# Kernel tuning notes

Measured on AMD Instinct MI355X. Metric: run time of the kernel, lower is better.

Reference implementation:

```python
import jax, jax.numpy as jnp
import numpy as np

N_NODES = 100000


def gcn_conv(x, edge_index, W, b):
    # PyG GCNConv: add self-loops, symmetric normalization, then scatter-add.
    n = x.shape[0]
    loops = jnp.arange(n, dtype=edge_index.dtype)
    src = jnp.concatenate([edge_index[0], loops])
    dst = jnp.concatenate([edge_index[1], loops])
    h = x @ W  # [N, F_out] -- transform before propagate (small GEMM)
    ones = jnp.ones(src.shape[0], dtype=x.dtype)
    deg = jax.ops.segment_sum(ones, dst, num_segments=n)  # in-degree incl. self-loop
    dinv = jnp.where(deg > 0, jax.lax.rsqrt(deg), 0.0)
    norm = dinv[src] * dinv[dst]  # [E+N]
    msg = h[src] * norm[:, None]  # gather + scale, [E+N, F_out]
    out = jax.ops.segment_sum(msg, dst, num_segments=n)  # scatter-add
    return out + b


def setup_inputs() -> dict:
    key = jax.random.key(0)
    k1, k2, k3, k4 = jax.random.split(key, 4)
    d = 128
    x = jax.random.normal(k1, (N_NODES, d), dtype=jnp.float32)
    edge_index = jax.random.randint(k2, (2, 1600000), 0, N_NODES, dtype=jnp.int64)
    scale = 1.0 / np.sqrt(d)
    W1 = jax.random.normal(k3, (d, d), dtype=jnp.float32) * scale
    b1 = jnp.zeros((d,), dtype=jnp.float32)
    W2 = jax.random.normal(k4, (d, d), dtype=jnp.float32) * scale
    b2 = jnp.zeros((d,), dtype=jnp.float32)
    return {"x": x, "edge_index": edge_index, "W1": W1, "b1": b1, "W2": W2, "b2": b2}


def reference(x, edge_index, W1, b1, W2, b2):
    # Layer 1: GCNConv -> relu -> dropout(eval: identity)
    h = jax.nn.relu(gcn_conv(x, edge_index, W1, b1))
    # Layer 2
    h = jax.nn.relu(gcn_conv(h, edge_index, W2, b2))
    return h
```

## Files before the change

kernel.cpp:

```cpp
#include <hip/hip_runtime.h>


#define NFEAT 128
#define BSH 7
#define MAXNB 1024
#define BCAP 4096
#define HP 72
#define YP 132
#define CH2 2048
#define CLCAP 2064

typedef __attribute__((ext_vector_type(8))) short s8v;
typedef __attribute__((ext_vector_type(4))) float f4v;
typedef __attribute__((ext_vector_type(2))) float f2v;
typedef __attribute__((ext_vector_type(4))) uint u4v;

__device__ inline ushort f2bf(float f) {
    union { float f; uint u; } x; x.f = f;
    uint u = x.u;
    return (ushort)((u + 0x7fffu + ((u >> 16) & 1u)) >> 16);
}
__device__ inline f2v unpk(uint u) {
    union { uint u; float f; } lo, hi;
    lo.u = u << 16;
    hi.u = u & 0xffff0000u;
    return (f2v){lo.f, hi.f};
}
__device__ inline void upadd2(uint4 v, f2v* a) {
    a[0] += unpk(v.x);
    a[1] += unpk(v.y);
    a[2] += unpk(v.z);
    a[3] += unpk(v.w);
}

__device__ inline void node_gather_lds(const uint4* __restrict__ hs4,
                                       const int* colL, int s, int e,
                                       int node, int sub, f2v* a) {
    uint4 vself = hs4[(size_t)node * 16 + sub];
    int nb = (e - s) >> 2;
    int k = s;
    if (nb > 0) {
        int c0 = colL[k], c1 = colL[k + 1], c2 = colL[k + 2], c3 = colL[k + 3];
        uint4 v0 = hs4[(size_t)c0 * 16 + sub];
        uint4 v1 = hs4[(size_t)c1 * 16 + sub];
        uint4 v2 = hs4[(size_t)c2 * 16 + sub];
        uint4 v3 = hs4[(size_t)c3 * 16 + sub];
        int d0 = colL[k + 4], d1 = colL[k + 5], d2 = colL[k + 6], d3 = colL[k + 7];
        k += 8;
        upadd2(vself, a);
        for (int it = 1; it < nb; ++it, k += 4) {
            uint4 w0 = hs4[(size_t)d0 * 16 + sub];
            uint4 w1 = hs4[(size_t)d1 * 16 + sub];
            uint4 w2 = hs4[(size_t)d2 * 16 + sub];
            uint4 w3 = hs4[(size_t)d3 * 16 + sub];
            int t0 = colL[k], t1 = colL[k + 1], t2 = colL[k + 2], t3 = colL[k + 3];
            upadd2(v0, a); upadd2(v1, a); upadd2(v2, a); upadd2(v3, a);
            v0 = w0; v1 = w1; v2 = w2; v3 = w3;
            d0 = t0; d1 = t1; d2 = t2; d3 = t3;
        }
        upadd2(v0, a); upadd2(v1, a); upadd2(v2, a); upadd2(v3, a);
        k = s + nb * 4;
    } else {
        upadd2(vself, a);
    }
    for (; k < e; ++k) upadd2(hs4[(size_t)colL[k] * 16 + sub], a);
}

__device__ inline void half_sort(const uint* __restrict__ ebuf,
                                 const int* __restrict__ gcnt,
                                 int b, int half, int* cnt, int* sstart, int* pre,
                                 int* colL) {
    int t = threadIdx.x;
    int m = min(gcnt[b], BCAP);
    const uint* eb = ebuf + (size_t)b * BCAP;
    if (t < 64) cnt[t] = 0;
    __syncthreads();
    for (int i = t; i < m; i += 256) {
        int low = (int)(eb[i] & 127u);
        if ((low >> 6) == half) atomicAdd(&cnt[low & 63], 1);
    }
    __syncthreads();
    if (t < 64) {
        int v = cnt[t];
        int sc = v;
#pragma unroll
        for (int off = 1; off < 64; off <<= 1) {
            int u = __shfl_up(sc, off, 64);
            if (t >= off) sc += u;
        }
        sstart[t] = sc - v;
        pre[t] = sc - v;
    }
    __syncthreads();
    for (int i = t; i < m; i += 256) {
        uint p = eb[i];
        int low = (int)(p & 127u);
        if ((low >> 6) == half) {
            int pos = atomicAdd(&pre[low & 63], 1);
            if (pos < 2048) colL[pos] = (int)(p >> BSH);
        }
    }
    __syncthreads();
}

__device__ inline void stage_w_half(ushort* Bs, const float* __restrict__ W, int h, int t) {
#pragma unroll
    for (int i = 0; i < 8; i++) {
        int idx = t + i * 256;
        int k4 = idx >> 7;
        int n = idx & 127;
        ushort o[4];
#pragma unroll
        for (int j = 0; j < 4; j++) o[j] = f2bf(W[(h * 64 + k4 * 4 + j) * NFEAT + n]);
        uint2 pk;
        __builtin_memcpy(&pk, o, 8);
        *(uint2*)&Bs[n * HP + k4 * 4] = pk;
    }
}

__global__ __launch_bounds__(256) void k_deg(const int* __restrict__ dst,
                                             int* __restrict__ deg, int E) {
    int i = blockIdx.x * 256 + threadIdx.x;
    int stride = gridDim.x * 256;
    int E4 = E >> 2;
    const int4* d4 = (const int4*)dst;
    for (int k = i; k < E4; k += stride) {
        int4 v = d4[k];
        atomicAdd(&deg[v.x], 1);
        atomicAdd(&deg[v.y], 1);
        atomicAdd(&deg[v.z], 1);
        atomicAdd(&deg[v.w], 1);
    }
    for (int k = E4 * 4 + i; k < E; k += stride) atomicAdd(&deg[dst[k]], 1);
}

__device__ inline void bsort_body(char* smem, int sid,
                                  const int* __restrict__ src,
                                  const int* __restrict__ dst,
                                  int* __restrict__ gcnt,
                                  uint* __restrict__ ebuf, int E, int NB) {
    int* cnt_ = (int*)smem;
    int* loff = cnt_ + MAXNB;
    int* gbase = loff + MAXNB;
    int* wpart = gbase + MAXNB;
    uint* sv = (uint*)(wpart + 4);
    ushort* sb = (ushort*)(sv + CH2);

    int t = threadIdx.x;
    int e0 = sid * CH2;
    int m = min(CH2, E - e0);

#pragma unroll
    for (int i = t; i < MAXNB; i += 256) cnt_[i] = 0;
    __syncthreads();
    for (int e = e0 + t; e < e0 + m; e += 256) atomicAdd(&cnt_[dst[e] >> BSH], 1);
    __syncthreads();
    for (int b = t; b < NB; b += 256) {
        int c = cnt_[b];
        gbase[b] = c ? (b * BCAP + atomicAdd(&gcnt[b], c)) : 0;
    }
    int v0 = cnt_[t * 4], v1 = cnt_[t * 4 + 1], v2 = cnt_[t * 4 + 2], v3 = cnt_[t * 4 + 3];
    int my = v0 + v1 + v2 + v3;
    int lane = t & 63, wv = t >> 6;
    int sc = my;
#pragma unroll
    for (int off = 1; off < 64; off <<= 1) {
        int up = __shfl_up(sc, off, 64);
        if (lane >= off) sc += up;
    }
    if (lane == 63) wpart[wv] = sc;
    __syncthreads();
    int wbase = 0;
    for (int j = 0; j < wv; j++) wbase += wpart[j];
    int run = wbase + sc - my;
    loff[t * 4] = run; cnt_[t * 4] = run; run += v0;
    loff[t * 4 + 1] = run; cnt_[t * 4 + 1] = run; run += v1;
    loff[t * 4 + 2] = run; cnt_[t * 4 + 2] = run; run += v2;
    loff[t * 4 + 3] = run; cnt_[t * 4 + 3] = run;
    __syncthreads();
    for (int e = e0 + t; e < e0 + m; e += 256) {
        int d = dst[e];
        int b = d >> BSH;
        int p = atomicAdd(&cnt_[b], 1);
        sv[p] = ((uint)src[e] << BSH) | (uint)(d & ((1 << BSH) - 1));
        sb[p] = (ushort)b;
    }
    __syncthreads();
    for (int i = t; i < m; i += 256) {
        int b = sb[i];
        int slot = gbase[b] + (i - loff[b]);
        if (slot < (b + 1) * BCAP) ebuf[slot] = sv[i];
    }
}

__device__ inline void gemm_body_f32(ushort* Bs, int bid, const float* __restrict__ Ap,
                                     const float* __restrict__ W,
                                     const int* __restrict__ deg,
                                     ushort* __restrict__ hs, int M) {
    int t = threadIdx.x;
    int w = t >> 6, l = t & 63;
    int q = l >> 4, ln = l & 15;
    int row0 = (bid * 4 + w) * 16;

    int arow = row0 + ln;
    if (arow >= M) arow = M - 1;
    s8v afr[4];
    const float* A = Ap + (size_t)arow * NFEAT + q * 8;
#pragma unroll
    for (int g = 0; g < 4; g++) {
        float4 f0 = *(const float4*)(A + g * 32);
        float4 f1 = *(const float4*)(A + g * 32 + 4);
        ushort o[8] = {f2bf(f0.x), f2bf(f0.y), f2bf(f0.z), f2bf(f0.w),
                       f2bf(f1.x), f2bf(f1.y), f2bf(f1.z), f2bf(f1.w)};
        __builtin_memcpy(&afr[g], o, 16);
    }

    f4v acc[8];
#pragma unroll
    for (int nt = 0; nt < 8; nt++) acc[nt] = (f4v){0.f, 0.f, 0.f, 0.f};

#pragma unroll
    for (int h = 0; h < 2; h++) {
        if (h) __syncthreads();
        stage_w_half(Bs, W, h, t);
        __syncthreads();
#pragma unroll
        for (int nt = 0; nt < 8; nt++) {
            const ushort* Bp = Bs + (nt * 16 + ln) * HP + q * 8;
#pragma unroll
            for (int ks = 0; ks < 2; ks++) {
                s8v bfr = *(const s8v*)(Bp + ks * 32);
                acc[nt] = __builtin_amdgcn_mfma_f32_16x16x32_bf16(afr[h * 2 + ks], bfr, acc[nt], 0, 0, 0);
            }
        }
    }

#pragma unroll
    for (int r = 0; r < 4; r++) {
        int row = row0 + q * 4 + r;
        if (row < M) {
            float sc = rsqrtf((float)(deg[row] + 1));
            ushort* hp = hs + (size_t)row * NFEAT + ln;
#pragma unroll
            for (int nt = 0; nt < 8; nt++) hp[nt * 16] = f2bf(acc[nt][r] * sc);
        }
    }
}

__global__ __launch_bounds__(256) void k_fusedA(const int* __restrict__ src,
                                                const int* __restrict__ dst,
                                                int* __restrict__ gcnt,
                                                uint* __restrict__ ebuf,
                                                int E, int NB, int chBlk,
                                                const float* __restrict__ x,
                                                const float* __restrict__ W1,
                                                const int* __restrict__ deg,
                                                ushort* __restrict__ hs, int M) {
    __shared__ __align__(16) char smem[24592];
    int bid = blockIdx.x;
    int sid = bid / 3, r = bid % 3;
    if (r == 0 && sid < chBlk) {
        bsort_body(smem, sid, src, dst, gcnt, ebuf, E, NB);
    } else {
        int sorts_before = min(sid + (r ? 1 : 0), chBlk);
        gemm_body_f32((ushort*)smem, bid - sorts_before, x, W1, deg, hs, M);
    }
}

__global__ __launch_bounds__(256, 4) void k_aggB1(const uint4* __restrict__ hs4,
                                                  const uint* __restrict__ ebuf,
                                                  const int* __restrict__ gcnt,
                                                  const float* __restrict__ bias,
                                                  const float* __restrict__ W2,
                                                  ushort* __restrict__ hs2, int N) {
    __shared__ __align__(16) char smem[36096];
    ushort* yT = (ushort*)smem;
    char* scr = smem + 16896;
    int* cnt = (int*)(smem + 35328);
    int* sstart = (int*)(smem + 35584);
    int* pre = (int*)(smem + 35840);
    int* colL = (int*)scr;
    ushort* Bs = (ushort*)scr;

    int t = threadIdx.x;
    int b = blockIdx.x >> 1, half = blockIdx.x & 1;
    int base = (b << BSH) + half * 64;

    half_sort(ebuf, gcnt, b, half, cnt, sstart, pre, colL);

    int grp = t >> 4, sub = t & 15;
    const float4* b4 = (const float4*)bias;
    float4 bb0 = b4[sub * 2], bb1 = b4[sub * 2 + 1];

    for (int i = 0; i < 4; i++) {
        int lo = grp + i * 16;
        int node = base + lo;
        uint4 pk = make_uint4(0, 0, 0, 0);
        if (node < N) {
            f2v a[4];
#pragma unroll
            for (int j = 0; j < 4; j++) a[j] = (f2v){0.f, 0.f};
            int s = sstart[lo];
            int e = min(s + cnt[lo], 2048);
            node_gather_lds(hs4, colL, s, e, node, sub, a);
            float di = rsqrtf((float)(cnt[lo] + 1));
            ushort o[8];
            o[0] = f2bf(fmaxf(fmaf(di, a[0].x, bb0.x), 0.f));
            o[1] = f2bf(fmaxf(fmaf(di, a[0].y, bb0.y), 0.f));
            o[2] = f2bf(fmaxf(fmaf(di, a[1].x, bb0.z), 0.f));
            o[3] = f2bf(fmaxf(fmaf(di, a[1].y, bb0.w), 0.f));
            o[4] = f2bf(fmaxf(fmaf(di, a[2].x, bb1.x), 0.f));
            o[5] = f2bf(fmaxf(fmaf(di, a[2].y, bb1.y), 0.f));
            o[6] = f2bf(fmaxf(fmaf(di, a[3].x, bb1.z), 0.f));
            o[7] = f2bf(fmaxf(fmaf(di, a[3].y, bb1.w), 0.f));
            __builtin_memcpy(&pk, o, 16);
        }
        *(uint4*)&yT[lo * YP + sub * 8] = pk;
    }
    __syncthreads();

    int w = t >> 6, l = t & 63;
    int q = l >> 4, ln = l & 15;
    s8v a2[4];
#pragma unroll
    for (int g = 0; g < 4; g++)
        a2[g] = *(const s8v*)&yT[(w * 16 + ln) * YP + g * 32 + q * 8];

    f4v acc[8];
#pragma unroll
    for (int nt = 0; nt < 8; nt++) acc[nt] = (f4v){0.f, 0.f, 0.f, 0.f};
#pragma unroll
    for (int h = 0; h < 2; h++) {
        if (h) __syncthreads();
        stage_w_half(Bs, W2, h, t);
        __syncthreads();
#pragma unroll
        for (int nt = 0; nt < 8; nt++) {
            const ushort* Bp = Bs + (nt * 16 + ln) * HP + q * 8;
#pragma unroll
            for (int ks = 0; ks < 2; ks++) {
                s8v bfr = *(const s8v*)(Bp + ks * 32);
                acc[nt] = __builtin_amdgcn_mfma_f32_16x16x32_bf16(a2[h * 2 + ks], bfr, acc[nt], 0, 0, 0);
            }
        }
    }
#pragma unroll
    for (int rr = 0; rr < 4; rr++) {
        int lrow = w * 16 + q * 4 + rr;
        int node = base + lrow;
        if (node < N) {
            float sc = rsqrtf((float)(cnt[lrow] + 1));
            ushort* hp = hs2 + (size_t)node * NFEAT + ln;
#pragma unroll
            for (int nt = 0; nt < 8; nt++) hp[nt * 16] = f2bf(acc[nt][rr] * sc);
        }
    }
}

__global__ __launch_bounds__(256, 6) void k_aggB2(const uint4* __restrict__ hs4,
                                                  const uint* __restrict__ ebuf,
                                                  const int* __restrict__ gcnt,
                                                  const float* __restrict__ bias,
                                                  float* __restrict__ outp, int N) {
    __shared__ int cnt[64];
    __shared__ int sstart[64];
    __shared__ int pre[64];
    __shared__ int colL[CLCAP];

    int t = threadIdx.x;
    int b = blockIdx.x >> 1, half = blockIdx.x & 1;
    int base = (b << BSH) + half * 64;

    half_sort(ebuf, gcnt, b, half, cnt, sstart, pre, colL);

    int grp = t >> 4, sub = t & 15;
    const float4* b4 = (const float4*)bias;
    float4 bb0 = b4[sub * 2], bb1 = b4[sub * 2 + 1];

    for (int i = 0; i < 4; i++) {
        int lo = grp + i * 16;
        int node = base + lo;
        if (node >= N) continue;
        f2v a[4];
#pragma unroll
        for (int j = 0; j < 4; j++) a[j] = (f2v){0.f, 0.f};
        int s = sstart[lo];
        int e = min(s + cnt[lo], 2048);
        node_gather_lds(hs4, colL, s, e, node, sub, a);
        float di = rsqrtf((float)(cnt[lo] + 1));
        float r[8];
        r[0] = fmaxf(fmaf(di, a[0].x, bb0.x), 0.f);
        r[1] = fmaxf(fmaf(di, a[0].y, bb0.y), 0.f);
        r[2] = fmaxf(fmaf(di, a[1].x, bb0.z), 0.f);
        r[3] = fmaxf(fmaf(di, a[1].y, bb0.w), 0.f);
        r[4] = fmaxf(fmaf(di, a[2].x, bb1.x), 0.f);
        r[5] = fmaxf(fmaf(di, a[2].y, bb1.y), 0.f);
        r[6] = fmaxf(fmaf(di, a[3].x, bb1.z), 0.f);
        r[7] = fmaxf(fmaf(di, a[3].y, bb1.w), 0.f);
        float* orow = outp + (size_t)node * NFEAT + sub * 8;
        f4v r0 = {r[0], r[1], r[2], r[3]};
        f4v r1 = {r[4], r[5], r[6], r[7]};
        __builtin_nontemporal_store(r0, (f4v*)orow);
        __builtin_nontemporal_store(r1, (f4v*)(orow + 4));
    }
}

extern "C" void kernel_launch(void* const* d_in, const int* in_sizes, int n_in,
                              void* d_out, int out_size, void* d_ws, size_t ws_size,
                              hipStream_t stream) {
    const float* x = (const float*)d_in[0];
    const int* ei = (const int*)d_in[1];
    const float* W1 = (const float*)d_in[2];
    const float* b1 = (const float*)d_in[3];
    const float* W2 = (const float*)d_in[4];
    const float* b2 = (const float*)d_in[5];
    float* out = (float*)d_out;

    const int N = in_sizes[0] / NFEAT;
    const int E = in_sizes[1] / 2;
    const int* src = ei;
    const int* dst = ei + E;
    const int NB = (N + (1 << BSH) - 1) >> BSH;

    char* w = (char*)d_ws;
    size_t off = 0;
    auto alloc = [&](size_t bytes) -> void* {
        void* p = w + off;
        off = (off + bytes + 511) & ~(size_t)511;
        return p;
    };
    ushort* hs = (ushort*)alloc((size_t)N * NFEAT * 2);
    ushort* hs2 = (ushort*)alloc((size_t)N * NFEAT * 2);
    int* deg = (int*)alloc((size_t)N * 4);
    uint* ebuf = (uint*)alloc((size_t)NB * BCAP * 4);
    int* gcnt = (int*)alloc((size_t)MAXNB * 4);
    (void)ws_size; (void)n_in; (void)out_size;

    const int sortBlk = (E + CH2 - 1) / CH2;
    const int gemmBlk = (N + 63) / 64;
    const int aggBlk = 2 * NB;

    hipMemsetAsync(deg, 0, (size_t)N * 4, stream);
    hipMemsetAsync(gcnt, 0, (size_t)MAXNB * 4, stream);
    k_deg<<<1024, 256, 0, stream>>>(dst, deg, E);
    k_fusedA<<<sortBlk + gemmBlk, 256, 0, stream>>>(src, dst, gcnt, ebuf, E, NB, sortBlk,
                                                    x, W1, deg, hs, N);
    k_aggB1<<<aggBlk, 256, 0, stream>>>((const uint4*)hs, ebuf, gcnt, b1, W2, hs2, N);
    k_aggB2<<<aggBlk, 256, 0, stream>>>((const uint4*)hs2, ebuf, gcnt, b2, out, N);
}
```

Before: 357.9 us.

## Fuse degree count into sort, apply source norm at gather, reuse sorted columns

```diff
diff --git a/kernel.cpp b/kernel.cpp
--- a/kernel.cpp
+++ b/kernel.cpp
@@ -7,13 +7,12 @@
 #define BCAP 4096
 #define HP 72
 #define YP 132
-#define CH2 2048
-#define CLCAP 2064
+#define CH2 8192
+#define SEG 2048
 
 typedef __attribute__((ext_vector_type(8))) short s8v;
 typedef __attribute__((ext_vector_type(4))) float f4v;
 typedef __attribute__((ext_vector_type(2))) float f2v;
-typedef __attribute__((ext_vector_type(4))) uint u4v;
 
 __device__ inline ushort f2bf(float f) {
     union { float f; uint u; } x; x.f = f;
@@ -26,44 +25,51 @@
     hi.u = u & 0xffff0000u;
     return (f2v){lo.f, hi.f};
 }
-__device__ inline void upadd2(uint4 v, f2v* a) {
-    a[0] += unpk(v.x);
-    a[1] += unpk(v.y);
-    a[2] += unpk(v.z);
-    a[3] += unpk(v.w);
-}
-
-__device__ inline void node_gather_lds(const uint4* __restrict__ hs4,
-                                       const int* colL, int s, int e,
-                                       int node, int sub, f2v* a) {
+__device__ inline void upfma2(uint4 v, float g, f2v* a) {
+    a[0] += g * unpk(v.x);
+    a[1] += g * unpk(v.y);
+    a[2] += g * unpk(v.z);
+    a[3] += g * unpk(v.w);
+}
+
+__device__ inline void node_gather2(const uint4* __restrict__ hs4,
+                                    const int* col, const float* __restrict__ dinv,
+                                    int s, int e, int node, int sub, f2v* a) {
     uint4 vself = hs4[(size_t)node * 16 + sub];
+    float dself = dinv[node];
     int nb = (e - s) >> 2;
     int k = s;
     if (nb > 0) {
-        int c0 = colL[k], c1 = colL[k + 1], c2 = colL[k + 2], c3 = colL[k + 3];
+        int c0 = col[k], c1 = col[k + 1], c2 = col[k + 2], c3 = col[k + 3];
         uint4 v0 = hs4[(size_t)c0 * 16 + sub];
         uint4 v1 = hs4[(size_t)c1 * 16 + sub];
         uint4 v2 = hs4[(size_t)c2 * 16 + sub];
         uint4 v3 = hs4[(size_t)c3 * 16 + sub];
-        int d0 = colL[k + 4], d1 = colL[k + 5], d2 = colL[k + 6], d3 = colL[k + 7];
+        float g0 = dinv[c0], g1 = dinv[c1], g2 = dinv[c2], g3 = dinv[c3];
+        int d0 = col[k + 4], d1 = col[k + 5], d2 = col[k + 6], d3 = col[k + 7];
         k += 8;
-        upadd2(vself, a);
+        upfma2(vself, dself, a);
         for (int it = 1; it < nb; ++it, k += 4) {
             uint4 w0 = hs4[(size_t)d0 * 16 + sub];
             uint4 w1 = hs4[(size_t)d1 * 16 + sub];
             uint4 w2 = hs4[(size_t)d2 * 16 + sub];
             uint4 w3 = hs4[(size_t)d3 * 16 + sub];
-            int t0 = colL[k], t1 = colL[k + 1], t2 = colL[k + 2], t3 = colL[k + 3];
-            upadd2(v0, a); upadd2(v1, a); upadd2(v2, a); upadd2(v3, a);
+            float h0 = dinv[d0], h1 = dinv[d1], h2 = dinv[d2], h3 = dinv[d3];
+            int t0 = col[k], t1 = col[k + 1], t2 = col[k + 2], t3 = col[k + 3];
+            upfma2(v0, g0, a); upfma2(v1, g1, a); upfma2(v2, g2, a); upfma2(v3, g3, a);
             v0 = w0; v1 = w1; v2 = w2; v3 = w3;
+            g0 = h0; g1 = h1; g2 = h2; g3 = h3;
             d0 = t0; d1 = t1; d2 = t2; d3 = t3;
         }
-        upadd2(v0, a); upadd2(v1, a); upadd2(v2, a); upadd2(v3, a);
+        upfma2(v0, g0, a); upfma2(v1, g1, a); upfma2(v2, g2, a); upfma2(v3, g3, a);
         k = s + nb * 4;
     } else {
-        upadd2(vself, a);
-    }
-    for (; k < e; ++k) upadd2(hs4[(size_t)colL[k] * 16 + sub], a);
+        upfma2(vself, dself, a);
+    }
+    for (; k < e; ++k) {
+        int c = col[k];
+        upfma2(hs4[(size_t)c * 16 + sub], dinv[c], a);
+    }
 }
 
 __device__ inline void half_sort(const uint* __restrict__ ebuf,
@@ -97,7 +103,7 @@
         int low = (int)(p & 127u);
         if ((low >> 6) == half) {
             int pos = atomicAdd(&pre[low & 63], 1);
-            if (pos < 2048) colL[pos] = (int)(p >> BSH);
+            if (pos < SEG) colL[pos] = (int)(p >> BSH);
         }
     }
     __syncthreads();
@@ -118,32 +124,32 @@
     }
 }
 
-__global__ __launch_bounds__(256) void k_deg(const int* __restrict__ dst,
-                                             int* __restrict__ deg, int E) {
-    int i = blockIdx.x * 256 + threadIdx.x;
-    int stride = gridDim.x * 256;
-    int E4 = E >> 2;
-    const int4* d4 = (const int4*)dst;
-    for (int k = i; k < E4; k += stride) {
-        int4 v = d4[k];
-        atomicAdd(&deg[v.x], 1);
-        atomicAdd(&deg[v.y], 1);
-        atomicAdd(&deg[v.z], 1);
-        atomicAdd(&deg[v.w], 1);
-    }
-    for (int k = E4 * 4 + i; k < E; k += stride) atomicAdd(&deg[dst[k]], 1);
+__device__ inline void stage_w_half512(ushort* Bs, const float* __restrict__ W, int h, int t) {
+#pragma unroll
+    for (int i = 0; i < 4; i++) {
+        int idx = t + i * 512;
+        int k4 = idx >> 7;
+        int n = idx & 127;
+        ushort o[4];
+#pragma unroll
+        for (int j = 0; j < 4; j++) o[j] = f2bf(W[(h * 64 + k4 * 4 + j) * NFEAT + n]);
+        uint2 pk;
+        __builtin_memcpy(&pk, o, 8);
+        *(uint2*)&Bs[n * HP + k4 * 4] = pk;
+    }
 }
 
 __device__ inline void bsort_body(char* smem, int sid,
                                   const int* __restrict__ src,
                                   const int* __restrict__ dst,
                                   int* __restrict__ gcnt,
+                                  int* __restrict__ deg,
                                   uint* __restrict__ ebuf, int E, int NB) {
     int* cnt_ = (int*)smem;
     int* loff = cnt_ + MAXNB;
     int* gbase = loff + MAXNB;
     int* wpart = gbase + MAXNB;
-    uint* sv = (uint*)(wpart + 4);
+    uint* sv = (uint*)(wpart + 8);
     ushort* sb = (ushort*)(sv + CH2);
 
     int t = threadIdx.x;
@@ -151,16 +157,20 @@
     int m = min(CH2, E - e0);
 
 #pragma unroll
-    for (int i = t; i < MAXNB; i += 256) cnt_[i] = 0;
-    __syncthreads();
-    for (int e = e0 + t; e < e0 + m; e += 256) atomicAdd(&cnt_[dst[e] >> BSH], 1);
-    __syncthreads();
-    for (int b = t; b < NB; b += 256) {
+    for (int i = t; i < MAXNB; i += 512) cnt_[i] = 0;
+    __syncthreads();
+    for (int e = e0 + t; e < e0 + m; e += 512) {
+        int d = dst[e];
+        atomicAdd(&cnt_[d >> BSH], 1);
+        atomicAdd(&deg[d], 1);
+    }
+    __syncthreads();
+    for (int b = t; b < NB; b += 512) {
         int c = cnt_[b];
         gbase[b] = c ? (b * BCAP + atomicAdd(&gcnt[b], c)) : 0;
     }
-    int v0 = cnt_[t * 4], v1 = cnt_[t * 4 + 1], v2 = cnt_[t * 4 + 2], v3 = cnt_[t * 4 + 3];
-    int my = v0 + v1 + v2 + v3;
+    int v0 = cnt_[t * 2], v1 = cnt_[t * 2 + 1];
+    int my = v0 + v1;
     int lane = t & 63, wv = t >> 6;
     int sc = my;
 #pragma unroll
@@ -171,14 +181,13 @@
     if (lane == 63) wpart[wv] = sc;
     __syncthreads();
     int wbase = 0;
-    for (int j = 0; j < wv; j++) wbase += wpart[j];
+#pragma unroll
+    for (int j = 0; j < 8; j++) wbase += (j < wv) ? wpart[j] : 0;
     int run = wbase + sc - my;
-    loff[t * 4] = run; cnt_[t * 4] = run; run += v0;
-    loff[t * 4 + 1] = run; cnt_[t * 4 + 1] = run; run += v1;
-    loff[t * 4 + 2] = run; cnt_[t * 4 + 2] = run; run += v2;
-    loff[t * 4 + 3] = run; cnt_[t * 4 + 3] = run;
-    __syncthreads();
-    for (int e = e0 + t; e < e0 + m; e += 256) {
+    loff[t * 2] = run; cnt_[t * 2] = run; run += v0;
+    loff[t * 2 + 1] = run; cnt_[t * 2 + 1] = run;
+    __syncthreads();
+    for (int e = e0 + t; e < e0 + m; e += 512) {
         int d = dst[e];
         int b = d >> BSH;
         int p = atomicAdd(&cnt_[b], 1);
@@ -186,26 +195,25 @@
         sb[p] = (ushort)b;
     }
     __syncthreads();
-    for (int i = t; i < m; i += 256) {
+    for (int i = t; i < m; i += 512) {
         int b = sb[i];
         int slot = gbase[b] + (i - loff[b]);
         if (slot < (b + 1) * BCAP) ebuf[slot] = sv[i];
     }
 }
 
-__device__ inline void gemm_body_f32(ushort* Bs, int bid, const float* __restrict__ Ap,
-                                     const float* __restrict__ W,
-                                     const int* __restrict__ deg,
-                                     ushort* __restrict__ hs, int M) {
+__device__ inline void gemm_body512(ushort* Bs, int gid, const float* __restrict__ x,
+                                    const float* __restrict__ W,
+                                    ushort* __restrict__ hs, int M) {
     int t = threadIdx.x;
     int w = t >> 6, l = t & 63;
     int q = l >> 4, ln = l & 15;
-    int row0 = (bid * 4 + w) * 16;
+    int row0 = (gid * 8 + w) * 16;
 
     int arow = row0 + ln;
     if (arow >= M) arow = M - 1;
     s8v afr[4];
-    const float* A = Ap + (size_t)arow * NFEAT + q * 8;
+    const float* A = x + (size_t)arow * NFEAT + q * 8;
 #pragma unroll
     for (int g = 0; g < 4; g++) {
         float4 f0 = *(const float4*)(A + g * 32);
@@ -222,7 +230,7 @@
 #pragma unroll
     for (int h = 0; h < 2; h++) {
         if (h) __syncthreads();
-        stage_w_half(Bs, W, h, t);
+        stage_w_half512(Bs, W, h, t);
         __syncthreads();
 #pragma unroll
         for (int nt = 0; nt < 8; nt++) {
@@ -239,39 +247,46 @@
     for (int r = 0; r < 4; r++) {
         int row = row0 + q * 4 + r;
         if (row < M) {
-            float sc = rsqrtf((float)(deg[row] + 1));
             ushort* hp = hs + (size_t)row * NFEAT + ln;
 #pragma unroll
-            for (int nt = 0; nt < 8; nt++) hp[nt * 16] = f2bf(acc[nt][r] * sc);
-        }
-    }
-}
-
-__global__ __launch_bounds__(256) void k_fusedA(const int* __restrict__ src,
+            for (int nt = 0; nt < 8; nt++) hp[nt * 16] = f2bf(acc[nt][r]);
+        }
+    }
+}
+
+__global__ __launch_bounds__(512) void k_fusedA(const int* __restrict__ src,
                                                 const int* __restrict__ dst,
                                                 int* __restrict__ gcnt,
+                                                int* __restrict__ deg,
                                                 uint* __restrict__ ebuf,
-                                                int E, int NB, int chBlk,
+                                                int E, int NB, int sortBlk,
                                                 const float* __restrict__ x,
                                                 const float* __restrict__ W1,
-                                                const int* __restrict__ deg,
                                                 ushort* __restrict__ hs, int M) {
-    __shared__ __align__(16) char smem[24592];
+    __shared__ __align__(16) char smem[61472];
     int bid = blockIdx.x;
-    int sid = bid / 3, r = bid % 3;
-    if (r == 0 && sid < chBlk) {
-        bsort_body(smem, sid, src, dst, gcnt, ebuf, E, NB);
+    int sid = bid / 5, r = bid % 5;
+    if (r == 0 && sid < sortBlk) {
+        bsort_body(smem, sid, src, dst, gcnt, deg, ebuf, E, NB);
     } else {
-        int sorts_before = min(sid + (r ? 1 : 0), chBlk);
-        gemm_body_f32((ushort*)smem, bid - sorts_before, x, W1, deg, hs, M);
-    }
-}
-
-__global__ __launch_bounds__(256, 4) void k_aggB1(const uint4* __restrict__ hs4,
+        int sorts_before = min((bid + 4) / 5, sortBlk);
+        gemm_body512((ushort*)smem, bid - sorts_before, x, W1, hs, M);
+    }
+}
+
+__global__ __launch_bounds__(256) void k_dinv(const int* __restrict__ deg,
+                                              float* __restrict__ dinv, int N) {
+    int i = blockIdx.x * 256 + threadIdx.x;
+    if (i < N) dinv[i] = rsqrtf((float)(deg[i] + 1));
+}
+
+__global__ __launch_bounds__(256, 4) void k_aggGS(const uint4* __restrict__ hs4,
                                                   const uint* __restrict__ ebuf,
                                                   const int* __restrict__ gcnt,
+                                                  const float* __restrict__ dinv,
                                                   const float* __restrict__ bias,
                                                   const float* __restrict__ W2,
+                                                  int* __restrict__ col2,
                                                   ushort* __restrict__ hs2, int N) {
     __shared__ __align__(16) char smem[36096];
     ushort* yT = (ushort*)smem;
@@ -283,10 +298,15 @@
     ushort* Bs = (ushort*)scr;
 
     int t = threadIdx.x;
-    int b = blockIdx.x >> 1, half = blockIdx.x & 1;
+    int hb = blockIdx.x;
+    int b = hb >> 1, half = hb & 1;
     int base = (b << BSH) + half * 64;
 
     half_sort(ebuf, gcnt, b, half, cnt, sstart, pre, colL);
+
+    int m2 = min(sstart[63] + cnt[63], SEG);
+    int* seg = col2 + (size_t)hb * SEG;
+    for (int i = t; i < m2; i += 256) seg[i] = colL[i];
 
     int grp = t >> 4, sub = t & 15;
     const float4* b4 = (const float4*)bias;
@@ -301,9 +321,9 @@
 #pragma unroll
             for (int j = 0; j < 4; j++) a[j] = (f2v){0.f, 0.f};
             int s = sstart[lo];
-            int e = min(s + cnt[lo], 2048);
-            node_gather_lds(hs4, colL, s, e, node, sub, a);
-            float di = rsqrtf((float)(cnt[lo] + 1));
+            int e = min(s + cnt[lo], SEG);
+            node_gather2(hs4, colL, dinv, s, e, node, sub, a);
+            float di = dinv[node];
             ushort o[8];
             o[0] = f2bf(fmaxf(fmaf(di, a[0].x, bb0.x), 0.f));
             o[1] = f2bf(fmaxf(fmaf(di, a[0].y, bb0.y), 0.f));
@@ -325,6 +345,7 @@
 #pragma unroll
     for (int g = 0; g < 4; g++)
         a2[g] = *(const s8v*)&yT[(w * 16 + ln) * YP + g * 32 + q * 8];
+    __syncthreads();
 
     f4v acc[8];
 #pragma unroll
@@ -346,34 +367,43 @@
     }
 #pragma unroll
     for (int rr = 0; rr < 4; rr++) {
-        int lrow = w * 16 + q * 4 + rr;
-        int node = base + lrow;
+        int node = base + w * 16 + q * 4 + rr;
         if (node < N) {
-            float sc = rsqrtf((float)(cnt[lrow] + 1));
             ushort* hp = hs2 + (size_t)node * NFEAT + ln;
 #pragma unroll
-            for (int nt = 0; nt < 8; nt++) hp[nt * 16] = f2bf(acc[nt][rr] * sc);
-        }
-    }
-}
-
-__global__ __launch_bounds__(256, 6) void k_aggB2(const uint4* __restrict__ hs4,
-                                                  const uint* __restrict__ ebuf,
-                                                  const int* __restrict__ gcnt,
-                                                  const float* __restrict__ bias,
-                                                  float* __restrict__ outp, int N) {
-    __shared__ int cnt[64];
+            for (int nt = 0; nt < 8; nt++) hp[nt * 16] = f2bf(acc[nt][rr]);
+        }
+    }
+}
+
+__global__ __launch_bounds__(256) void k_agg2(const uint4* __restrict__ hs4,
+                                              const int* __restrict__ col2,
+                                              const int* __restrict__ deg,
+                                              const float* __restrict__ dinv,
+                                              const float* __restrict__ bias,
+                                              float* __restrict__ outp, int N) {
     __shared__ int sstart[64];
-    __shared__ int pre[64];
-    __shared__ int colL[CLCAP];
-
+    __shared__ int scnt[64];
     int t = threadIdx.x;
-    int b = blockIdx.x >> 1, half = blockIdx.x & 1;
-    int base = (b << BSH) + half * 64;
-
-    half_sort(ebuf, gcnt, b, half, cnt, sstart, pre, colL);
+    int hb = blockIdx.x;
+    int base = ((hb >> 1) << BSH) + (hb & 1) * 64;
+
+    if (t < 64) {
+        int node = base + t;
+        int d = (node < N) ? deg[node] : 0;
+        int sc = d;
+#pragma unroll
+        for (int off = 1; off < 64; off <<= 1) {
+            int u = __shfl_up(sc, off, 64);
+            if (t >= off) sc += u;
+        }
+        sstart[t] = sc - d;
+        scnt[t] = d;
+    }
+    __syncthreads();
 
     int grp = t >> 4, sub = t & 15;
+    const int* seg = col2 + (size_t)hb * SEG;
     const float4* b4 = (const float4*)bias;
     float4 bb0 = b4[sub * 2], bb1 = b4[sub * 2 + 1];
 
@@ -384,10 +414,10 @@
         f2v a[4];
 #pragma unroll
         for (int j = 0; j < 4; j++) a[j] = (f2v){0.f, 0.f};
-        int s = sstart[lo];
-        int e = min(s + cnt[lo], 2048);
-        node_gather_lds(hs4, colL, s, e, node, sub, a);
-        float di = rsqrtf((float)(cnt[lo] + 1));
+        int s = min(sstart[lo], SEG);
+        int e = min(sstart[lo] + scnt[lo], SEG);
+        node_gather2(hs4, seg, dinv, s, e, node, sub, a);
+        float di = dinv[node];
         float r[8];
         r[0] = fmaxf(fmaf(di, a[0].x, bb0.x), 0.f);
         r[1] = fmaxf(fmaf(di, a[0].y, bb0.y), 0.f);
@@ -432,19 +462,22 @@
     ushort* hs = (ushort*)alloc((size_t)N * NFEAT * 2);
     ushort* hs2 = (ushort*)alloc((size_t)N * NFEAT * 2);
     int* deg = (int*)alloc((size_t)N * 4);
+    float* dinv = (float*)alloc((size_t)N * 4);
     uint* ebuf = (uint*)alloc((size_t)NB * BCAP * 4);
+    int* col2 = (int*)alloc(((size_t)2 * NB * SEG + 64) * 4);
     int* gcnt = (int*)alloc((size_t)MAXNB * 4);
     (void)ws_size; (void)n_in; (void)out_size;
 
     const int sortBlk = (E + CH2 - 1) / CH2;
-    const int gemmBlk = (N + 63) / 64;
+    const int gemmBlk = (N + 127) / 128;
     const int aggBlk = 2 * NB;
 
     hipMemsetAsync(deg, 0, (size_t)N * 4, stream);
     hipMemsetAsync(gcnt, 0, (size_t)MAXNB * 4, stream);
-    k_deg<<<1024, 256, 0, stream>>>(dst, deg, E);
-    k_fusedA<<<sortBlk + gemmBlk, 256, 0, stream>>>(src, dst, gcnt, ebuf, E, NB, sortBlk,
-                                                    x, W1, deg, hs, N);
-    k_aggB1<<<aggBlk, 256, 0, stream>>>((const uint4*)hs, ebuf, gcnt, b1, W2, hs2, N);
-    k_aggB2<<<aggBlk, 256, 0, stream>>>((const uint4*)hs2, ebuf, gcnt, b2, out, N);
-}
+    k_fusedA<<<sortBlk + gemmBlk, 512, 0, stream>>>(src, dst, gcnt, deg, ebuf, E, NB,
+                                                    sortBlk, x, W1, hs, N);
+    k_dinv<<<(N + 255) / 256, 256, 0, stream>>>(deg, dinv, N);
+    k_aggGS<<<aggBlk, 256, 0, stream>>>((const uint4*)hs, ebuf, gcnt, dinv, b1, W2,
+                                        col2, hs2, N);
+    k_agg2<<<aggBlk, 256, 0, stream>>>((const uint4*)hs2, col2, deg, dinv, b2, out, N);
+}
```

Result: faster. 347.4 us (-2.9%).
